# Optimization experiments

Measured on AMD Instinct MI355X. Metric: run time of the kernel, lower is better.

## Reference

```python
import jax, jax.numpy as jnp
import numpy as np

CUTOFF = 10.0
K = 32            # max_num_neighbors
NUM_GRAPHS = 64
ATOMS = 128
N = NUM_GRAPHS * ATOMS
HID = 128
FIL = 128
NG = 50           # num_gaussians
LAYERS = 6
MAX_Z = 100
PI = 3.14159265   # constant used verbatim in the torch source


def silu(x):
    return x * jax.nn.sigmoid(x)


def build_graph(pos, batch):
    """Dense cdist + per-node top-K neighbor selection (radius_graph_pure).
    Returns idx[i,k] = k-th nearest neighbor j of center i, and a validity mask.
    Torch edge (row, col) = (j, i): node j receives a message computed from x[i].
    """
    p = jax.lax.stop_gradient(pos)
    d2 = jnp.sum((p[:, None, :] - p[None, :, :]) ** 2, -1)          # [N,N]
    same = batch[:, None] == batch[None, :]
    eye = jnp.eye(p.shape[0], dtype=bool)
    valid = same & (d2 < CUTOFF * CUTOFF) & (~eye)
    dm = jnp.where(valid, d2, jnp.inf)
    neg, idx = jax.lax.top_k(-dm, K)                                 # [N,K]
    return idx, jnp.isfinite(neg)                                    # edge valid iff within mask


def setup_inputs() -> dict:
    key = jax.random.key(0)
    ks = jax.random.split(key, 20)
    s = 0.05
    inp = {
        "pos": jax.random.normal(ks[0], (N, 3), jnp.float32),
        "z": jax.random.randint(ks[1], (N,), 0, MAX_Z),
        "batch": jnp.repeat(jnp.arange(NUM_GRAPHS), ATOMS),
        # parameters (weights stored as [in, out])
        "emb": jax.random.normal(ks[2], (MAX_Z, HID), jnp.float32) * s,
        "mw1": jax.random.normal(ks[3], (LAYERS, NG, FIL), jnp.float32) * s,
        "mb1": jax.random.normal(ks[4], (LAYERS, FIL), jnp.float32) * s,
        "mw2": jax.random.normal(ks[5], (LAYERS, FIL, FIL), jnp.float32) * s,
        "mb2": jax.random.normal(ks[6], (LAYERS, FIL), jnp.float32) * s,
        "l1w": jax.random.normal(ks[7], (LAYERS, HID, FIL), jnp.float32) * s,
        "l1b": jax.random.normal(ks[8], (LAYERS, FIL), jnp.float32) * s,
        "l2w": jax.random.normal(ks[9], (LAYERS, FIL, HID), jnp.float32) * s,
        "l2b": jax.random.normal(ks[10], (LAYERS, HID), jnp.float32) * s,
        "ow1": jax.random.normal(ks[11], (HID, HID // 2), jnp.float32) * s,
        "ob1": jax.random.normal(ks[12], (HID // 2,), jnp.float32) * s,
        "ow2": jax.random.normal(ks[13], (HID // 2, 1), jnp.float32) * s,
        "ob2": jax.random.normal(ks[14], (1,), jnp.float32) * s,
    }
    return inp


def reference(pos, z, batch, emb, mw1, mb1, mw2, mb2, l1w, l1b, l2w, l2b, ow1, ob1, ow2, ob2):
    idx, evalid = build_graph(pos, batch)                 # [N,K], [N,K]
    ev = evalid.astype(pos.dtype)
    diff = pos[idx] - pos[:, None, :]                     # [N,K,3]
    d2e = jnp.sum(diff * diff, -1)
    dist = jnp.sqrt(jnp.where(evalid, d2e, 1.0))          # safe sqrt for masked edges
    offset = jnp.linspace(0.0, CUTOFF, NG)
    width = CUTOFF / (NG - 1)
    rbf = jnp.exp(-0.5 * ((dist[..., None] - offset) / width) ** 2)   # [N,K,NG]
    cval = 0.5 * (jnp.cos(dist * PI / CUTOFF) + 1.0)
    cval = cval * (dist < CUTOFF).astype(pos.dtype) * ev  # zero out invalid edges

    h = emb[z]                                            # [N,HID]
    flat_idx = idx.reshape(-1)                            # receivers (torch row)
    for l in range(LAYERS):
        W = silu(rbf @ mw1[l] + mb1[l]) @ mw2[l] + mb2[l]           # filter MLP
        W = W * cval[..., None]                                       # [N,K,FIL]
        xj = (h @ l1w[l] + l1b[l])[:, None, :]                        # sender = center i
        msg = (xj * W).reshape(N * K, FIL)
        agg = jax.ops.segment_sum(msg, flat_idx, num_segments=N)     # scatter_add at row
        h = h + silu(agg @ l2w[l] + l2b[l])

    out = (silu(h @ ow1 + ob1) @ ow2 + ob2)[:, 0]         # [N]
    return jax.ops.segment_sum(out, batch, num_segments=NUM_GRAPHS)  # [G]
```

## Files before the change

kernel.cpp:

```cpp
#include <hip/hip_runtime.h>
#include <math.h>

typedef unsigned short u16;
typedef unsigned int   u32;
typedef unsigned long long u64;

#define NATOMS 8192
#define GRAPHS 64
#define APG    128
#define KNN    32
#define NGAUSS 50
#define HID    128
#define LAYERS 6
#define NTAB   4096
#define SA     136
#define SW1    72
#define SH     132

typedef __attribute__((ext_vector_type(8))) short bf16x8;
typedef __attribute__((ext_vector_type(4))) float f32x4;

__device__ __forceinline__ float bf2f(u16 v) {
    return __uint_as_float(((u32)v) << 16);
}
__device__ __forceinline__ u16 f2bf(float f) {
    u32 u = __float_as_uint(f);
    u32 lsb = (u >> 16) & 1u;
    u += 0x7fffu + lsb;
    return (u16)(u >> 16);
}
__device__ __forceinline__ u32 pkbf(float lo, float hi) {
#if __has_builtin(__builtin_amdgcn_cvt_pk_bf16_f32)
    auto r = __builtin_amdgcn_cvt_pk_bf16_f32(lo, hi);
    u32 u; __builtin_memcpy(&u, &r, 4); return u;
#else
    return (u32)f2bf(lo) | ((u32)f2bf(hi) << 16);
#endif
}
__device__ __forceinline__ float silu_f(float x) {
    return x * __builtin_amdgcn_rcpf(1.0f + __expf(-x));
}
__device__ __forceinline__ bf16x8 ldfrag(const u16* p) {
    return *(const bf16x8*)__builtin_assume_aligned(p, 16);
}
__device__ __forceinline__ u64 shfl_xor_u64(u64 v, int mask) {
    u32 lo = (u32)v, hi = (u32)(v >> 32);
    lo = (u32)__shfl_xor((int)lo, mask, 64);
    hi = (u32)__shfl_xor((int)hi, mask, 64);
    return ((u64)hi << 32) | lo;
}
union U8 { bf16x8 v; u32 w[4]; };

__global__ void probe_kernel(const u16* __restrict__ raw, int* __restrict__ flag,
                             int* __restrict__ rev_cnt, float* __restrict__ gsum) {
    __shared__ int s;
    int t = threadIdx.x;
    if (t == 0) s = 0;
    __syncthreads();
    float x = bf2f(raw[2 * t]);
    if (!(fabsf(x) < 1000.0f)) atomicOr(&s, 1);
    for (int i = t; i < NATOMS; i += 256) rev_cnt[i] = 0;
    if (t < GRAPHS) gsum[t] = 0.0f;
    __syncthreads();
    if (t == 0) *flag = s;
}

#define NARR 10
struct IngestDesc {
    const void* src[NARR];
    void*       dst[NARR];
    int         n[NARR];
};

__global__ void ingest_kernel(IngestDesc d, const int* __restrict__ flag, int total) {
    int gid = blockIdx.x * blockDim.x + threadIdx.x;
    if (gid >= total) return;
    int a = 0, off = gid;
    while (off >= d.n[a]) { off -= d.n[a]; ++a; }
    bool f32in = (*flag != 0);
    float v = f32in ? ((const float*)d.src[a])[off]
                    : bf2f(((const u16*)d.src[a])[off]);
    ((float*)d.dst[a])[off] = v;
}

__global__ void prep_weights(const void* __restrict__ l1w, const void* __restrict__ l2w,
                             const void* __restrict__ mw2, const void* __restrict__ mw1,
                             u16* __restrict__ l1wt, u16* __restrict__ l2wt,
                             u16* __restrict__ mw2t, u16* __restrict__ mw1t,
                             const int* __restrict__ flag) {
    int gid = blockIdx.x * blockDim.x + threadIdx.x;
    bool f32in = (*flag != 0);
    if (gid < 3 * 98304) {
        int seg = gid / 98304;
        int t = gid % 98304;
        int l = t >> 14;
        int n = (t >> 7) & 127;
        int k = t & 127;
        const void* src = (seg == 0) ? l1w : ((seg == 1) ? l2w : mw2);
        u16* dst = (seg == 0) ? l1wt : ((seg == 1) ? l2wt : mw2t);
        int si = l * 16384 + k * 128 + n;
        float v = f32in ? ((const float*)src)[si] : bf2f(((const u16*)src)[si]);
        dst[t] = f2bf(v);
    } else {
        int t = gid - 3 * 98304;
        if (t < 49152) {
            int l = t >> 13;
            int n = (t >> 6) & 127;
            int k = t & 63;
            float v = 0.0f;
            if (k < 50) {
                int si = l * 6400 + k * 128 + n;
                v = f32in ? ((const float*)mw1)[si] : bf2f(((const u16*)mw1)[si]);
            }
            mw1t[t] = f2bf(v);
        }
    }
}

__launch_bounds__(256)
__global__ void build_graph_kernel(const float* __restrict__ pos,
                                   int* __restrict__ rev_cnt,
                                   int2* __restrict__ rev_si) {
    int wv = threadIdx.x >> 6, lane = threadIdx.x & 63;
    int t = blockIdx.x * 4 + wv;
    int tl = t & 127;
    int base = t & ~127;
    float cx = pos[t * 3 + 0];
    float cy = pos[t * 3 + 1];
    float cz = pos[t * 3 + 2];
    u64 key[2];
#pragma unroll
    for (int c = 0; c < 2; ++c) {
        int j = lane + c * 64;
        float jx = pos[(base + j) * 3 + 0];
        float jy = pos[(base + j) * 3 + 1];
        float jz = pos[(base + j) * 3 + 2];
        float dx = __fsub_rn(cx, jx);
        float dy = __fsub_rn(cy, jy);
        float dz = __fsub_rn(cz, jz);
        float d2 = __fadd_rn(__fadd_rn(__fmul_rn(dx, dx), __fmul_rn(dy, dy)),
                             __fmul_rn(dz, dz));
        bool valid = (j != tl) && (d2 < 100.0f);
        key[c] = valid ? ((((u64)__float_as_uint(d2)) << 32) | (u32)j) : ~0ULL;
    }
#pragma unroll
    for (int k = 2; k <= 128; k <<= 1) {
#pragma unroll
        for (int j = k >> 1; j > 0; j >>= 1) {
            if (j == 64) {
                u64 lo = key[0] < key[1] ? key[0] : key[1];
                u64 hi = key[0] < key[1] ? key[1] : key[0];
                key[0] = lo; key[1] = hi;
            } else {
#pragma unroll
                for (int r = 0; r < 2; ++r) {
                    u64 o = shfl_xor_u64(key[r], j);
                    u32 ii = (u32)(r * 64 + lane);
                    bool dir = ((ii & (u32)k) == 0);
                    bool lower = ((ii & (u32)j) == 0);
                    bool keep_min = (dir == lower);
                    bool less = key[r] < o;
                    key[r] = (less == keep_min) ? key[r] : o;
                }
            }
        }
    }
    if (lane < KNN) {
        u64 m = key[0];
        if (m != ~0ULL) {
            float d2 = __uint_as_float((u32)(m >> 32));
            float d = __fsqrt_rn(d2);
            if (d < 10.0f) {
                float u = d * ((float)(NTAB - 1) / 10.0f);
                int i0 = (int)(u + 0.5f);
                if (i0 > NTAB - 1) i0 = NTAB - 1;
                int jn = base + (int)(m & 0xffffffffu);
                int p = atomicAdd(&rev_cnt[jn], 1);
                rev_si[(size_t)jn * 128 + p] = make_int2(t, i0);
            }
        }
    }
}

__launch_bounds__(256)
__global__ void vtab_kernel(const u16* __restrict__ mw1t,
                            const u16* __restrict__ mw2t,
                            const float* __restrict__ b1,
                            const float* __restrict__ b2,
                            u32* __restrict__ pk) {
    __shared__ u16 s_t1[128 * SA];
    __shared__ u16 s_w1[128 * SW1];
    __shared__ u16 s_w2[128 * SA];
    int tid = threadIdx.x;
    int l = blockIdx.x / (NTAB / 128);
    int rbase = (blockIdx.x % (NTAB / 128)) * 128;
    {
        const uint4* g1 = (const uint4*)(mw1t + (size_t)l * 8192);
#pragma unroll
        for (int p = 0; p < 4; ++p) {
            int q = tid + p * 256;
            int row = q >> 3, c8 = (q & 7) * 8;
            *(uint4*)&s_w1[row * SW1 + c8] = g1[q];
        }
        const uint4* g2 = (const uint4*)(mw2t + (size_t)l * 16384);
#pragma unroll
        for (int p = 0; p < 8; ++p) {
            int q = tid + p * 256;
            int row = q >> 4, c8 = (q & 15) * 8;
            *(uint4*)&s_w2[row * SA + c8] = g2[q];
        }
    }
    __syncthreads();

    int wv = tid >> 6, lane = tid & 63;
    int quad = lane >> 4, lr = lane & 15;
    int m0 = wv * 32;

    {
        const float wgi = 49.0f / 10.0f;
        const float dstep = 10.0f / (float)(NTAB - 1);
        U8 afr[2][2];
#pragma unroll
        for (int mt = 0; mt < 2; ++mt) {
            float d = (float)(rbase + m0 + mt * 16 + lr) * dstep;
            float u = d * wgi;
#pragma unroll
            for (int kki = 0; kki < 2; ++kki) {
                float t0 = u - (float)(quad * 8) - (float)(kki * 32);
                float vj[8];
#pragma unroll
                for (int j = 0; j < 8; ++j) {
                    float tt = t0 - (float)j;
                    float e = __expf(-0.5f * tt * tt);
                    if (kki == 1 && (quad * 8 + j) >= 18) e = 0.0f;
                    vj[j] = e;
                }
#pragma unroll
                for (int p = 0; p < 4; ++p)
                    afr[mt][kki].w[p] = pkbf(vj[2 * p], vj[2 * p + 1]);
            }
        }
        f32x4 accA[2][8];
#pragma unroll
        for (int mt = 0; mt < 2; ++mt)
#pragma unroll
            for (int nt = 0; nt < 8; ++nt) accA[mt][nt] = (f32x4){0.f, 0.f, 0.f, 0.f};
#pragma unroll
        for (int kki = 0; kki < 2; ++kki) {
#pragma unroll
            for (int nt = 0; nt < 8; ++nt) {
                bf16x8 b = ldfrag(&s_w1[(nt * 16 + lr) * SW1 + kki * 32 + quad * 8]);
                accA[0][nt] = __builtin_amdgcn_mfma_f32_16x16x32_bf16(afr[0][kki].v, b, accA[0][nt], 0, 0, 0);
                accA[1][nt] = __builtin_amdgcn_mfma_f32_16x16x32_bf16(afr[1][kki].v, b, accA[1][nt], 0, 0, 0);
            }
        }
#pragma unroll
        for (int mt = 0; mt < 2; ++mt) {
            int r0 = m0 + mt * 16 + quad * 4;
            u16* tp0 = &s_t1[r0 * SA + lr];
#pragma unroll
            for (int nt = 0; nt < 8; ++nt) {
                int col = nt * 16;
                float bb = b1[l * 128 + col + lr];
                u32 p01 = pkbf(silu_f(accA[mt][nt][0] + bb),
                               silu_f(accA[mt][nt][1] + bb));
                u32 p23 = pkbf(silu_f(accA[mt][nt][2] + bb),
                               silu_f(accA[mt][nt][3] + bb));
                u16* tp = tp0 + col;
                tp[0]      = (u16)p01;
                tp[SA]     = (u16)(p01 >> 16);
                tp[2 * SA] = (u16)p23;
                tp[3 * SA] = (u16)(p23 >> 16);
            }
        }
    }

    {
        f32x4 accB[2][8];
#pragma unroll
        for (int mt = 0; mt < 2; ++mt)
#pragma unroll
            for (int nt = 0; nt < 8; ++nt) accB[mt][nt] = (f32x4){0.f, 0.f, 0.f, 0.f};
#pragma unroll
        for (int kk = 0; kk < 128; kk += 32) {
            bf16x8 a0 = ldfrag(&s_t1[(m0 + lr)      * SA + kk + quad * 8]);
            bf16x8 a1 = ldfrag(&s_t1[(m0 + 16 + lr) * SA + kk + quad * 8]);
#pragma unroll
            for (int nt = 0; nt < 8; ++nt) {
                bf16x8 b = ldfrag(&s_w2[(nt * 16 + lr) * SA + kk + quad * 8]);
                accB[0][nt] = __builtin_amdgcn_mfma_f32_16x16x32_bf16(a0, b, accB[0][nt], 0, 0, 0);
                accB[1][nt] = __builtin_amdgcn_mfma_f32_16x16x32_bf16(a1, b, accB[1][nt], 0, 0, 0);
            }
        }
        const float dstep = 10.0f / (float)(NTAB - 1);
#pragma unroll
        for (int mt = 0; mt < 2; ++mt) {
            int r0 = m0 + mt * 16 + quad * 4;
            float cv[4];
#pragma unroll
            for (int r = 0; r < 4; ++r) {
                float d = (float)(rbase + r0 + r) * dstep;
                cv[r] = 0.5f * (cosf(d * 3.14159265f / 10.0f) + 1.0f);
            }
#pragma unroll
            for (int nt = 0; nt < 8; ++nt) {
                int col = nt * 16 + lr;
                float bb = b2[l * 128 + col];
#pragma unroll
                for (int r = 0; r < 4; ++r) {
                    float val = (accB[mt][nt][r] + bb) * cv[r];
                    float oth = __shfl_xor(val, 1, 64);
                    if ((lr & 1) == 0) {
                        int row = rbase + r0 + r;
                        pk[((size_t)l * NTAB + row) * 64 + (col >> 1)] =
                            pkbf(val, oth);
                    }
                }
            }
        }
    }
}

__launch_bounds__(256)
__global__ void gemm0_kernel(const int* __restrict__ z,
                             const float* __restrict__ emb,
                             const u16* __restrict__ Bt,
                             const float* __restrict__ bias,
                             u16* __restrict__ xjb) {
    __shared__ u16 s_a[16 * SA];
    __shared__ float s_bias[128];
    int tid = threadIdx.x;
    int row0 = blockIdx.x * 16;
#pragma unroll
    for (int p = 0; p < 2; ++p) {
        int q = tid + p * 256;
        int r = q >> 5, c4 = (q & 31) * 4;
        const float* src = emb + (size_t)z[row0 + r] * 128;
        float4 v = *(const float4*)(src + c4);
        u32* d = (u32*)&s_a[r * SA + c4];
        d[0] = pkbf(v.x, v.y); d[1] = pkbf(v.z, v.w);
    }
    if (tid < 128) s_bias[tid] = bias[tid];
    __syncthreads();
    int wv = tid >> 6, lane = tid & 63;
    int quad = lane >> 4, lr = lane & 15;
    int n0 = wv * 32;
    f32x4 acc[2];
#pragma unroll
    for (int nt = 0; nt < 2; ++nt) acc[nt] = (f32x4){0.f, 0.f, 0.f, 0.f};
#pragma unroll
    for (int kk = 0; kk < 128; kk += 32) {
        bf16x8 a = ldfrag(&s_a[lr * SA + kk + quad * 8]);
#pragma unroll
        for (int nt = 0; nt < 2; ++nt) {
            bf16x8 b = ldfrag(Bt + (n0 + nt * 16 + lr) * 128 + kk + quad * 8);
            acc[nt] = __builtin_amdgcn_mfma_f32_16x16x32_bf16(a, b, acc[nt], 0, 0, 0);
        }
    }
#pragma unroll
    for (int nt = 0; nt < 2; ++nt)
#pragma unroll
        for (int r = 0; r < 4; ++r) {
            int col = n0 + nt * 16 + lr;
            xjb[(size_t)(row0 + quad * 4 + r) * 128 + col] =
                f2bf(acc[nt][r] + s_bias[col]);
        }
}

__launch_bounds__(256, 4)
__global__ void agg_kernel(const int* __restrict__ rev_cnt,
                           const int2* __restrict__ rev_si,
                           const u32* __restrict__ pk,
                           const u16* __restrict__ xjb,
                           float* __restrict__ agg) {
    int j = blockIdx.x * 4 + (threadIdx.x >> 6);
    int lane = threadIdx.x & 63;
    int deg = rev_cnt[j];
    const int2* si = rev_si + (size_t)j * 128;
    int c2 = lane * 2;
    float a0 = 0.f, a1 = 0.f, b0 = 0.f, b1 = 0.f;
    float c0 = 0.f, c1 = 0.f, d0 = 0.f, d1 = 0.f;
    int it = 0;
    for (; it + 8 <= deg; it += 8) {
        u32 t[8], x[8];
#pragma unroll
        for (int q = 0; q < 8; ++q) {
            int2 s = si[it + q];
            t[q] = pk[(size_t)s.y * 64 + lane];
            x[q] = *(const u32*)(xjb + (size_t)s.x * 128 + c2);
        }
#pragma unroll
        for (int q = 0; q < 8; ++q) {
            float v0 = bf2f((u16)t[q]) * bf2f((u16)x[q]);
            float v1 = bf2f((u16)(t[q] >> 16)) * bf2f((u16)(x[q] >> 16));
            switch (q & 3) {
                case 0: a0 += v0; a1 += v1; break;
                case 1: b0 += v0; b1 += v1; break;
                case 2: c0 += v0; c1 += v1; break;
                default: d0 += v0; d1 += v1; break;
            }
        }
    }
    for (; it + 4 <= deg; it += 4) {
        u32 t[4], x[4];
#pragma unroll
        for (int q = 0; q < 4; ++q) {
            int2 s = si[it + q];
            t[q] = pk[(size_t)s.y * 64 + lane];
            x[q] = *(const u32*)(xjb + (size_t)s.x * 128 + c2);
        }
#pragma unroll
        for (int q = 0; q < 4; ++q) {
            float v0 = bf2f((u16)t[q]) * bf2f((u16)x[q]);
            float v1 = bf2f((u16)(t[q] >> 16)) * bf2f((u16)(x[q] >> 16));
            if (q == 0) { a0 += v0; a1 += v1; }
            else if (q == 1) { b0 += v0; b1 += v1; }
            else if (q == 2) { c0 += v0; c1 += v1; }
            else { d0 += v0; d1 += v1; }
        }
    }
    for (; it < deg; ++it) {
        int2 s = si[it];
        u32 t = pk[(size_t)s.y * 64 + lane];
        u32 x = *(const u32*)(xjb + (size_t)s.x * 128 + c2);
        a0 += bf2f((u16)t) * bf2f((u16)x);
        a1 += bf2f((u16)(t >> 16)) * bf2f((u16)(x >> 16));
    }
    float2 r;
    r.x = (a0 + b0) + (c0 + d0);
    r.y = (a1 + b1) + (c1 + d1);
    *(float2*)(agg + (size_t)j * 128 + c2) = r;
}

template <int EMB, int LAST>
__launch_bounds__(256)
__global__ void layer_tail_kernel(const float* __restrict__ agg,
                                  float* __restrict__ h,
                                  const int* __restrict__ z,
                                  const float* __restrict__ emb,
                                  const u16* __restrict__ B2t,
                                  const float* __restrict__ b2,
                                  const u16* __restrict__ B1n,
                                  const float* __restrict__ b1n,
                                  u16* __restrict__ xjb) {
    __shared__ u16 s_ahi[16 * SA];
    __shared__ u16 s_alo[16 * SA];
    __shared__ float s_h[16 * SH];
    __shared__ float s_b2[128], s_b1[128];
    int tid = threadIdx.x;
    int row0 = blockIdx.x * 16;
#pragma unroll
    for (int p = 0; p < 2; ++p) {
        int q = tid + p * 256;
        int r = q >> 5, c4 = (q & 31) * 4;
        float4 v = *(const float4*)(agg + (size_t)(row0 + r) * 128 + c4);
        u32 h0 = pkbf(v.x, v.y), h1 = pkbf(v.z, v.w);
        u32* hd = (u32*)&s_ahi[r * SA + c4];
        hd[0] = h0; hd[1] = h1;
        u32 l0 = pkbf(v.x - bf2f((u16)h0), v.y - bf2f((u16)(h0 >> 16)));
        u32 l1 = pkbf(v.z - bf2f((u16)h1), v.w - bf2f((u16)(h1 >> 16)));
        u32* ld = (u32*)&s_alo[r * SA + c4];
        ld[0] = l0; ld[1] = l1;
    }
    if (tid < 128) {
        s_b2[tid] = b2[tid];
        if (!LAST) s_b1[tid] = b1n[tid];
    }
    __syncthreads();

    int wv = tid >> 6, lane = tid & 63;
    int quad = lane >> 4, lr = lane & 15;
    int n0 = wv * 32;

    f32x4 acc[2];
#pragma unroll
    for (int nt = 0; nt < 2; ++nt) acc[nt] = (f32x4){0.f, 0.f, 0.f, 0.f};
#pragma unroll
    for (int kk = 0; kk < 128; kk += 32) {
        bf16x8 ah = ldfrag(&s_ahi[lr * SA + kk + quad * 8]);
        bf16x8 al = ldfrag(&s_alo[lr * SA + kk + quad * 8]);
#pragma unroll
        for (int nt = 0; nt < 2; ++nt) {
            bf16x8 b = ldfrag(B2t + (n0 + nt * 16 + lr) * 128 + kk + quad * 8);
            acc[nt] = __builtin_amdgcn_mfma_f32_16x16x32_bf16(ah, b, acc[nt], 0, 0, 0);
            acc[nt] = __builtin_amdgcn_mfma_f32_16x16x32_bf16(al, b, acc[nt], 0, 0, 0);
        }
    }
#pragma unroll
    for (int nt = 0; nt < 2; ++nt)
#pragma unroll
        for (int r = 0; r < 4; ++r) {
            int row = quad * 4 + r;
            int col = n0 + nt * 16 + lr;
            size_t off = (size_t)(row0 + row) * 128 + col;
            float hold = EMB ? emb[(size_t)z[row0 + row] * 128 + col] : h[off];
            float hn = hold + silu_f(acc[nt][r] + s_b2[col]);
            h[off] = hn;
            s_h[row * SH + col] = hn;
        }
    if (!LAST) {
        __syncthreads();
        f32x4 ac2[2];
#pragma unroll
        for (int nt = 0; nt < 2; ++nt) ac2[nt] = (f32x4){0.f, 0.f, 0.f, 0.f};
#pragma unroll
        for (int kk = 0; kk < 128; kk += 32) {
            const float* ap = &s_h[lr * SH + kk + quad * 8];
            float4 v0 = *(const float4*)ap;
            float4 v1 = *(const float4*)(ap + 4);
            U8 a;
            a.w[0] = pkbf(v0.x, v0.y); a.w[1] = pkbf(v0.z, v0.w);
            a.w[2] = pkbf(v1.x, v1.y); a.w[3] = pkbf(v1.z, v1.w);
#pragma unroll
            for (int nt = 0; nt < 2; ++nt) {
                bf16x8 b = ldfrag(B1n + (n0 + nt * 16 + lr) * 128 + kk + quad * 8);
                ac2[nt] = __builtin_amdgcn_mfma_f32_16x16x32_bf16(a.v, b, ac2[nt], 0, 0, 0);
            }
        }
#pragma unroll
        for (int nt = 0; nt < 2; ++nt)
#pragma unroll
            for (int r = 0; r < 4; ++r) {
                int col = n0 + nt * 16 + lr;
                xjb[(size_t)(row0 + quad * 4 + r) * 128 + col] =
                    f2bf(ac2[nt][r] + s_b1[col]);
            }
    }
}

__launch_bounds__(256)
__global__ void head_kernel(const float* __restrict__ h,
                            const float* __restrict__ ow1,
                            const float* __restrict__ ob1,
                            const float* __restrict__ ow2,
                            const float* __restrict__ ob2,
                            float* __restrict__ gsum) {
    __shared__ __align__(16) float s_w[128 * 64];
    __shared__ __align__(16) float s_h[16 * 132];
    __shared__ float s_sum;
    int tid = threadIdx.x;
    int a0 = blockIdx.x * 16;
    if (tid == 0) s_sum = 0.0f;
    {
        const float4* src = (const float4*)ow1;
        float4* dst = (float4*)s_w;
#pragma unroll
        for (int p = 0; p < 8; ++p) dst[tid + p * 256] = src[tid + p * 256];
    }
    {
        const float4* src = (const float4*)(h + (size_t)a0 * 128);
#pragma unroll
        for (int p = 0; p < 2; ++p) {
            int q = tid + p * 256;
            int r = q >> 5, c4 = (q & 31) * 4;
            *(float4*)&s_h[r * 132 + c4] = src[q];
        }
    }
    __syncthreads();
    int atom = tid >> 4, cg = tid & 15;
    const float* hr = &s_h[atom * 132];
    const float4* w4 = (const float4*)s_w;
    float4 acc = {0.f, 0.f, 0.f, 0.f};
#pragma unroll 8
    for (int f = 0; f < 128; ++f) {
        float hv = hr[f];
        float4 w = w4[f * 16 + cg];
        acc.x += hv * w.x; acc.y += hv * w.y;
        acc.z += hv * w.z; acc.w += hv * w.w;
    }
    int c0 = cg * 4;
    float v = silu_f(acc.x + ob1[c0 + 0]) * ow2[c0 + 0]
            + silu_f(acc.y + ob1[c0 + 1]) * ow2[c0 + 1]
            + silu_f(acc.z + ob1[c0 + 2]) * ow2[c0 + 2]
            + silu_f(acc.w + ob1[c0 + 3]) * ow2[c0 + 3];
    v += __shfl_xor(v, 1, 64);
    v += __shfl_xor(v, 2, 64);
    v += __shfl_xor(v, 4, 64);
    v += __shfl_xor(v, 8, 64);
    if ((tid & 15) == 0) atomicAdd(&s_sum, v + ob2[0]);
    __syncthreads();
    if (tid == 0) atomicAdd(&gsum[a0 >> 7], s_sum);
}

__global__ void finalize_kernel(const float* __restrict__ gsum, void* __restrict__ out,
                                const int* __restrict__ flag) {
    int t = threadIdx.x;
    if (*flag) ((float*)out)[t] = gsum[t];
    else       ((u16*)out)[t]   = f2bf(gsum[t]);
}

extern "C" void kernel_launch(void* const* d_in, const int* in_sizes, int n_in,
                              void* d_out, int out_size, void* d_ws, size_t ws_size,
                              hipStream_t stream) {
    const void* pos  = d_in[0];
    const int*  z    = (const int*)d_in[1];
    const void* emb  = d_in[3];
    const void* mw1  = d_in[4];
    const void* mb1  = d_in[5];
    const void* mw2  = d_in[6];
    const void* mb2  = d_in[7];
    const void* l1w  = d_in[8];
    const void* l1b  = d_in[9];
    const void* l2w  = d_in[10];
    const void* l2b  = d_in[11];
    const void* ow1  = d_in[12];
    const void* ob1  = d_in[13];
    const void* ow2  = d_in[14];
    const void* ob2  = d_in[15];

    char* ws = (char*)d_ws;
    const size_t KB = 1024, MB = 1048576;
    int*   w_flag  = (int*)  (ws);
    float* c_pos   = (float*)(ws + 4   * KB);
    float* c_emb   = (float*)(ws + 112 * KB);
    float* c_mb1   = (float*)(ws + 168 * KB);
    float* c_mb2   = (float*)(ws + 176 * KB);
    float* c_l1b   = (float*)(ws + 184 * KB);
    float* c_l2b   = (float*)(ws + 192 * KB);
    float* c_ow1   = (float*)(ws + 200 * KB);
    float* c_ob1   = (float*)(ws + 236 * KB);
    float* c_ow2   = (float*)(ws + 240 * KB);
    float* c_ob2   = (float*)(ws + 244 * KB);
    float* w_gsum  = (float*)(ws + 248 * KB);
    u16*   c_l1wt  = (u16*)  (ws + 256 * KB);
    u16*   c_l2wt  = (u16*)  (ws + 448 * KB);
    u16*   c_mw2t  = (u16*)  (ws + 640 * KB);
    u16*   c_mw1t  = (u16*)  (ws + 832 * KB);
    int*   rev_cnt = (int*)  (ws + 2  * MB);
    int2*  rev_si  = (int2*) (ws + 3  * MB);
    float* w_h     = (float*)(ws + 11 * MB);
    u16*   w_xjb   = (u16*)  (ws + 15 * MB);
    float* w_agg   = (float*)(ws + 17 * MB);
    u32*   w_pk    = (u32*)  (ws + 21 * MB);

    probe_kernel<<<1, 256, 0, stream>>>((const u16*)emb, w_flag, rev_cnt, w_gsum);

    IngestDesc dsc;
    const void* srcs[NARR] = {pos, emb, mb1, mb2, l1b, l2b, ow1, ob1, ow2, ob2};
    void* dsts[NARR] = {c_pos, c_emb, c_mb1, c_mb2, c_l1b, c_l2b, c_ow1, c_ob1,
                        c_ow2, c_ob2};
    int ns_[NARR] = {24576, 12800, 768, 768, 768, 768, 8192, 64, 64, 1};
    int total = 0;
    for (int a = 0; a < NARR; ++a) {
        dsc.src[a] = srcs[a]; dsc.dst[a] = dsts[a]; dsc.n[a] = ns_[a];
        total += ns_[a];
    }
    ingest_kernel<<<(total + 255) / 256, 256, 0, stream>>>(dsc, w_flag, total);
    prep_weights<<<1344, 256, 0, stream>>>(l1w, l2w, mw2, mw1,
                                           c_l1wt, c_l2wt, c_mw2t, c_mw1t, w_flag);

    build_graph_kernel<<<NATOMS / 4, 256, 0, stream>>>(c_pos, rev_cnt, rev_si);
    vtab_kernel<<<LAYERS * NTAB / 128, 256, 0, stream>>>(
        c_mw1t, c_mw2t, c_mb1, c_mb2, w_pk);

    gemm0_kernel<<<NATOMS / 16, 256, 0, stream>>>(z, c_emb, c_l1wt, c_l1b, w_xjb);

    for (int l = 0; l < LAYERS; ++l) {
        agg_kernel<<<NATOMS / 4, 256, 0, stream>>>(
            rev_cnt, rev_si, w_pk + (size_t)l * NTAB * 64, w_xjb, w_agg);
        const u16* B2 = c_l2wt + (size_t)l * 16384;
        const float* b2 = c_l2b + (size_t)l * 128;
        const u16* B1n = c_l1wt + (size_t)(l + 1) * 16384;
        const float* b1n = c_l1b + (size_t)(l + 1) * 128;
        if (l == 0)
            layer_tail_kernel<1, 0><<<NATOMS / 16, 256, 0, stream>>>(
                w_agg, w_h, z, c_emb, B2, b2, B1n, b1n, w_xjb);
        else if (l < LAYERS - 1)
            layer_tail_kernel<0, 0><<<NATOMS / 16, 256, 0, stream>>>(
                w_agg, w_h, z, c_emb, B2, b2, B1n, b1n, w_xjb);
        else
            layer_tail_kernel<0, 1><<<NATOMS / 16, 256, 0, stream>>>(
                w_agg, w_h, z, c_emb, B2, b2, nullptr, nullptr, nullptr);
    }

    head_kernel<<<NATOMS / 16, 256, 0, stream>>>(w_h, c_ow1, c_ob1, c_ow2, c_ob2,
                                                 w_gsum);
    finalize_kernel<<<1, GRAPHS, 0, stream>>>(w_gsum, (void*)d_out, w_flag);
}
```

Baseline: 278.4 us.

## Fuse aggregation into layer tail, merge setup kernels, fold head and finalize

Merges ingest, weight prep and graph build into one setup kernel that reads pos directly. Each layer's gather-aggregate now runs inside the layer-tail GEMM kernel, so the fp32 agg buffer is never written to or read back from global memory. Ping-pong xjb buffers avoid read/write hazards. The output head and finalize step are folded into the last layer using a done-counter last-block pattern. This removes many launches and round trips, but the aggregation now runs with 512 blocks of 16 rows instead of 2048 blocks with one wave per node, which lowers parallelism for the latency-bound gather.

Result: slower. 295.6 us (+6.2%).

```diff
diff --git a/kernel.cpp b/kernel.cpp
--- a/kernel.cpp
+++ b/kernel.cpp
@@ -7,7 +7,6 @@
 
 #define NATOMS 8192
 #define GRAPHS 64
-#define APG    128
 #define KNN    32
 #define NGAUSS 50
 #define HID    128
@@ -49,10 +48,14 @@
     hi = (u32)__shfl_xor((int)hi, mask, 64);
     return ((u64)hi << 32) | lo;
 }
+__device__ __forceinline__ float ldf(const void* p, int i, bool f32in) {
+    return f32in ? ((const float*)p)[i] : bf2f(((const u16*)p)[i]);
+}
 union U8 { bf16x8 v; u32 w[4]; };
 
 __global__ void probe_kernel(const u16* __restrict__ raw, int* __restrict__ flag,
-                             int* __restrict__ rev_cnt, float* __restrict__ gsum) {
+                             int* __restrict__ rev_cnt, float* __restrict__ gsum,
+                             int* __restrict__ done_cnt) {
     __shared__ int s;
     int t = threadIdx.x;
     if (t == 0) s = 0;
@@ -61,123 +64,127 @@
     if (!(fabsf(x) < 1000.0f)) atomicOr(&s, 1);
     for (int i = t; i < NATOMS; i += 256) rev_cnt[i] = 0;
     if (t < GRAPHS) gsum[t] = 0.0f;
+    if (t == 0) *done_cnt = 0;
     __syncthreads();
     if (t == 0) *flag = s;
 }
 
-#define NARR 10
+#define NARR 9
 struct IngestDesc {
     const void* src[NARR];
     void*       dst[NARR];
     int         n[NARR];
 };
 
-__global__ void ingest_kernel(IngestDesc d, const int* __restrict__ flag, int total) {
-    int gid = blockIdx.x * blockDim.x + threadIdx.x;
-    if (gid >= total) return;
-    int a = 0, off = gid;
-    while (off >= d.n[a]) { off -= d.n[a]; ++a; }
-    bool f32in = (*flag != 0);
-    float v = f32in ? ((const float*)d.src[a])[off]
-                    : bf2f(((const u16*)d.src[a])[off]);
-    ((float*)d.dst[a])[off] = v;
-}
-
-__global__ void prep_weights(const void* __restrict__ l1w, const void* __restrict__ l2w,
+#define NB_BUILD 2048
+#define NB_PREP  1344
+
+__launch_bounds__(256)
+__global__ void setup_kernel(const void* __restrict__ pos,
+                             const void* __restrict__ l1w, const void* __restrict__ l2w,
                              const void* __restrict__ mw2, const void* __restrict__ mw1,
                              u16* __restrict__ l1wt, u16* __restrict__ l2wt,
                              u16* __restrict__ mw2t, u16* __restrict__ mw1t,
-                             const int* __restrict__ flag) {
-    int gid = blockIdx.x * blockDim.x + threadIdx.x;
+                             IngestDesc d, int total_ing,
+                             const int* __restrict__ flag,
+                             int* __restrict__ rev_cnt, int2* __restrict__ rev_si) {
+    int bid = blockIdx.x;
     bool f32in = (*flag != 0);
-    if (gid < 3 * 98304) {
-        int seg = gid / 98304;
-        int t = gid % 98304;
-        int l = t >> 14;
-        int n = (t >> 7) & 127;
-        int k = t & 127;
-        const void* src = (seg == 0) ? l1w : ((seg == 1) ? l2w : mw2);
-        u16* dst = (seg == 0) ? l1wt : ((seg == 1) ? l2wt : mw2t);
-        int si = l * 16384 + k * 128 + n;
-        float v = f32in ? ((const float*)src)[si] : bf2f(((const u16*)src)[si]);
-        dst[t] = f2bf(v);
+    if (bid < NB_BUILD) {
+        int wv = threadIdx.x >> 6, lane = threadIdx.x & 63;
+        int t = bid * 4 + wv;
+        int tl = t & 127;
+        int base = t & ~127;
+        float cx = ldf(pos, t * 3 + 0, f32in);
+        float cy = ldf(pos, t * 3 + 1, f32in);
+        float cz = ldf(pos, t * 3 + 2, f32in);
+        u64 key[2];
+#pragma unroll
+        for (int c = 0; c < 2; ++c) {
+            int j = lane + c * 64;
+            float jx = ldf(pos, (base + j) * 3 + 0, f32in);
+            float jy = ldf(pos, (base + j) * 3 + 1, f32in);
+            float jz = ldf(pos, (base + j) * 3 + 2, f32in);
+            float dx = __fsub_rn(cx, jx);
+            float dy = __fsub_rn(cy, jy);
+            float dz = __fsub_rn(cz, jz);
+            float d2 = __fadd_rn(__fadd_rn(__fmul_rn(dx, dx), __fmul_rn(dy, dy)),
+                                 __fmul_rn(dz, dz));
+            bool valid = (j != tl) && (d2 < 100.0f);
+            key[c] = valid ? ((((u64)__float_as_uint(d2)) << 32) | (u32)j) : ~0ULL;
+        }
+#pragma unroll
+        for (int k = 2; k <= 128; k <<= 1) {
+#pragma unroll
+            for (int j = k >> 1; j > 0; j >>= 1) {
+                if (j == 64) {
+                    u64 lo = key[0] < key[1] ? key[0] : key[1];
+                    u64 hi = key[0] < key[1] ? key[1] : key[0];
+                    key[0] = lo; key[1] = hi;
+                } else {
+#pragma unroll
+                    for (int r = 0; r < 2; ++r) {
+                        u64 o = shfl_xor_u64(key[r], j);
+                        u32 ii = (u32)(r * 64 + lane);
+                        bool dir = ((ii & (u32)k) == 0);
+                        bool lower = ((ii & (u32)j) == 0);
+                        bool keep_min = (dir == lower);
+                        bool less = key[r] < o;
+                        key[r] = (less == keep_min) ? key[r] : o;
+                    }
+                }
+            }
+        }
+        if (lane < KNN) {
+            u64 m = key[0];
+            if (m != ~0ULL) {
+                float d2 = __uint_as_float((u32)(m >> 32));
+                float dd = __fsqrt_rn(d2);
+                if (dd < 10.0f) {
+                    float u = dd * ((float)(NTAB - 1) / 10.0f);
+                    int i0 = (int)(u + 0.5f);
+                    if (i0 > NTAB - 1) i0 = NTAB - 1;
+                    int jn = base + (int)(m & 0xffffffffu);
+                    int p = atomicAdd(&rev_cnt[jn], 1);
+                    rev_si[(size_t)jn * 128 + p] = make_int2(t, i0);
+                }
+            }
+        }
+    } else if (bid < NB_BUILD + NB_PREP) {
+        int gid = (bid - NB_BUILD) * 256 + threadIdx.x;
+        if (gid < 3 * 98304) {
+            int seg = gid / 98304;
+            int tt = gid % 98304;
+            int l = tt >> 14;
+            int n = (tt >> 7) & 127;
+            int k = tt & 127;
+            const void* src = (seg == 0) ? l1w : ((seg == 1) ? l2w : mw2);
+            u16* dst = (seg == 0) ? l1wt : ((seg == 1) ? l2wt : mw2t);
+            int si = l * 16384 + k * 128 + n;
+            float v = f32in ? ((const float*)src)[si] : bf2f(((const u16*)src)[si]);
+            dst[tt] = f2bf(v);
+        } else {
+            int tt = gid - 3 * 98304;
+            if (tt < 49152) {
+                int l = tt >> 13;
+                int n = (tt >> 6) & 127;
+                int k = tt & 63;
+                float v = 0.0f;
+                if (k < 50) {
+                    int si = l * 6400 + k * 128 + n;
+                    v = f32in ? ((const float*)mw1)[si] : bf2f(((const u16*)mw1)[si]);
+                }
+                mw1t[tt] = f2bf(v);
+            }
+        }
     } else {
-        int t = gid - 3 * 98304;
-        if (t < 49152) {
-            int l = t >> 13;
-            int n = (t >> 6) & 127;
-            int k = t & 63;
-            float v = 0.0f;
-            if (k < 50) {
-                int si = l * 6400 + k * 128 + n;
-                v = f32in ? ((const float*)mw1)[si] : bf2f(((const u16*)mw1)[si]);
-            }
-            mw1t[t] = f2bf(v);
-        }
-    }
-}
-
-__launch_bounds__(256)
-__global__ void build_graph_kernel(const float* __restrict__ pos,
-                                   int* __restrict__ rev_cnt,
-                                   int2* __restrict__ rev_si) {
-    int wv = threadIdx.x >> 6, lane = threadIdx.x & 63;
-    int t = blockIdx.x * 4 + wv;
-    int tl = t & 127;
-    int base = t & ~127;
-    float cx = pos[t * 3 + 0];
-    float cy = pos[t * 3 + 1];
-    float cz = pos[t * 3 + 2];
-    u64 key[2];
-#pragma unroll
-    for (int c = 0; c < 2; ++c) {
-        int j = lane + c * 64;
-        float jx = pos[(base + j) * 3 + 0];
-        float jy = pos[(base + j) * 3 + 1];
-        float jz = pos[(base + j) * 3 + 2];
-        float dx = __fsub_rn(cx, jx);
-        float dy = __fsub_rn(cy, jy);
-        float dz = __fsub_rn(cz, jz);
-        float d2 = __fadd_rn(__fadd_rn(__fmul_rn(dx, dx), __fmul_rn(dy, dy)),
-                             __fmul_rn(dz, dz));
-        bool valid = (j != tl) && (d2 < 100.0f);
-        key[c] = valid ? ((((u64)__float_as_uint(d2)) << 32) | (u32)j) : ~0ULL;
-    }
-#pragma unroll
-    for (int k = 2; k <= 128; k <<= 1) {
-#pragma unroll
-        for (int j = k >> 1; j > 0; j >>= 1) {
-            if (j == 64) {
-                u64 lo = key[0] < key[1] ? key[0] : key[1];
-                u64 hi = key[0] < key[1] ? key[1] : key[0];
-                key[0] = lo; key[1] = hi;
-            } else {
-#pragma unroll
-                for (int r = 0; r < 2; ++r) {
-                    u64 o = shfl_xor_u64(key[r], j);
-                    u32 ii = (u32)(r * 64 + lane);
-                    bool dir = ((ii & (u32)k) == 0);
-                    bool lower = ((ii & (u32)j) == 0);
-                    bool keep_min = (dir == lower);
-                    bool less = key[r] < o;
-                    key[r] = (less == keep_min) ? key[r] : o;
-                }
-            }
-        }
-    }
-    if (lane < KNN) {
-        u64 m = key[0];
-        if (m != ~0ULL) {
-            float d2 = __uint_as_float((u32)(m >> 32));
-            float d = __fsqrt_rn(d2);
-            if (d < 10.0f) {
-                float u = d * ((float)(NTAB - 1) / 10.0f);
-                int i0 = (int)(u + 0.5f);
-                if (i0 > NTAB - 1) i0 = NTAB - 1;
-                int jn = base + (int)(m & 0xffffffffu);
-                int p = atomicAdd(&rev_cnt[jn], 1);
-                rev_si[(size_t)jn * 128 + p] = make_int2(t, i0);
-            }
+        int gid = (bid - NB_BUILD - NB_PREP) * 256 + threadIdx.x;
+        if (gid < total_ing) {
+            int a = 0, off = gid;
+            while (off >= d.n[a]) { off -= d.n[a]; ++a; }
+            float v = f32in ? ((const float*)d.src[a])[off]
+                            : bf2f(((const u16*)d.src[a])[off]);
+            ((float*)d.dst[a])[off] = v;
         }
     }
 }
@@ -274,7 +281,6 @@
             }
         }
     }
-
     {
         f32x4 accB[2][8];
 #pragma unroll
@@ -337,8 +343,8 @@
         int r = q >> 5, c4 = (q & 31) * 4;
         const float* src = emb + (size_t)z[row0 + r] * 128;
         float4 v = *(const float4*)(src + c4);
-        u32* d = (u32*)&s_a[r * SA + c4];
-        d[0] = pkbf(v.x, v.y); d[1] = pkbf(v.z, v.w);
+        u32* dd = (u32*)&s_a[r * SA + c4];
+        dd[0] = pkbf(v.x, v.y); dd[1] = pkbf(v.z, v.w);
     }
     if (tid < 128) s_bias[tid] = bias[tid];
     __syncthreads();
@@ -367,111 +373,118 @@
         }
 }
 
-__launch_bounds__(256, 4)
-__global__ void agg_kernel(const int* __restrict__ rev_cnt,
-                           const int2* __restrict__ rev_si,
-                           const u32* __restrict__ pk,
-                           const u16* __restrict__ xjb,
-                           float* __restrict__ agg) {
-    int j = blockIdx.x * 4 + (threadIdx.x >> 6);
-    int lane = threadIdx.x & 63;
-    int deg = rev_cnt[j];
-    const int2* si = rev_si + (size_t)j * 128;
-    int c2 = lane * 2;
-    float a0 = 0.f, a1 = 0.f, b0 = 0.f, b1 = 0.f;
-    float c0 = 0.f, c1 = 0.f, d0 = 0.f, d1 = 0.f;
-    int it = 0;
-    for (; it + 8 <= deg; it += 8) {
-        u32 t[8], x[8];
-#pragma unroll
-        for (int q = 0; q < 8; ++q) {
-            int2 s = si[it + q];
-            t[q] = pk[(size_t)s.y * 64 + lane];
-            x[q] = *(const u32*)(xjb + (size_t)s.x * 128 + c2);
-        }
-#pragma unroll
-        for (int q = 0; q < 8; ++q) {
-            float v0 = bf2f((u16)t[q]) * bf2f((u16)x[q]);
-            float v1 = bf2f((u16)(t[q] >> 16)) * bf2f((u16)(x[q] >> 16));
-            switch (q & 3) {
-                case 0: a0 += v0; a1 += v1; break;
-                case 1: b0 += v0; b1 += v1; break;
-                case 2: c0 += v0; c1 += v1; break;
-                default: d0 += v0; d1 += v1; break;
-            }
-        }
-    }
-    for (; it + 4 <= deg; it += 4) {
-        u32 t[4], x[4];
-#pragma unroll
-        for (int q = 0; q < 4; ++q) {
-            int2 s = si[it + q];
-            t[q] = pk[(size_t)s.y * 64 + lane];
-            x[q] = *(const u32*)(xjb + (size_t)s.x * 128 + c2);
-        }
-#pragma unroll
-        for (int q = 0; q < 4; ++q) {
-            float v0 = bf2f((u16)t[q]) * bf2f((u16)x[q]);
-            float v1 = bf2f((u16)(t[q] >> 16)) * bf2f((u16)(x[q] >> 16));
-            if (q == 0) { a0 += v0; a1 += v1; }
-            else if (q == 1) { b0 += v0; b1 += v1; }
-            else if (q == 2) { c0 += v0; c1 += v1; }
-            else { d0 += v0; d1 += v1; }
-        }
-    }
-    for (; it < deg; ++it) {
-        int2 s = si[it];
-        u32 t = pk[(size_t)s.y * 64 + lane];
-        u32 x = *(const u32*)(xjb + (size_t)s.x * 128 + c2);
-        a0 += bf2f((u16)t) * bf2f((u16)x);
-        a1 += bf2f((u16)(t >> 16)) * bf2f((u16)(x >> 16));
-    }
-    float2 r;
-    r.x = (a0 + b0) + (c0 + d0);
-    r.y = (a1 + b1) + (c1 + d1);
-    *(float2*)(agg + (size_t)j * 128 + c2) = r;
-}
-
 template <int EMB, int LAST>
 __launch_bounds__(256)
-__global__ void layer_tail_kernel(const float* __restrict__ agg,
-                                  float* __restrict__ h,
-                                  const int* __restrict__ z,
-                                  const float* __restrict__ emb,
-                                  const u16* __restrict__ B2t,
-                                  const float* __restrict__ b2,
-                                  const u16* __restrict__ B1n,
-                                  const float* __restrict__ b1n,
-                                  u16* __restrict__ xjb) {
+__global__ void layer_fused_kernel(const int* __restrict__ rev_cnt,
+                                   const int2* __restrict__ rev_si,
+                                   const u32* __restrict__ pk,
+                                   const u16* __restrict__ xjb_in,
+                                   float* __restrict__ h,
+                                   const int* __restrict__ z,
+                                   const float* __restrict__ emb,
+                                   const u16* __restrict__ B2t,
+                                   const float* __restrict__ b2,
+                                   const u16* __restrict__ B1n,
+                                   const float* __restrict__ b1n,
+                                   u16* __restrict__ xjb_out,
+                                   const float* __restrict__ ow1,
+                                   const float* __restrict__ ob1,
+                                   const float* __restrict__ ow2,
+                                   const float* __restrict__ ob2,
+                                   float* __restrict__ gsum,
+                                   int* __restrict__ done_cnt,
+                                   void* __restrict__ out,
+                                   const int* __restrict__ flag) {
     __shared__ u16 s_ahi[16 * SA];
     __shared__ u16 s_alo[16 * SA];
     __shared__ float s_h[16 * SH];
     __shared__ float s_b2[128], s_b1[128];
+    __shared__ float s_w[LAST ? 128 * 64 : 1];
+    __shared__ float s_sum;
+    __shared__ int s_last;
     int tid = threadIdx.x;
     int row0 = blockIdx.x * 16;
-#pragma unroll
-    for (int p = 0; p < 2; ++p) {
-        int q = tid + p * 256;
-        int r = q >> 5, c4 = (q & 31) * 4;
-        float4 v = *(const float4*)(agg + (size_t)(row0 + r) * 128 + c4);
-        u32 h0 = pkbf(v.x, v.y), h1 = pkbf(v.z, v.w);
-        u32* hd = (u32*)&s_ahi[r * SA + c4];
-        hd[0] = h0; hd[1] = h1;
-        u32 l0 = pkbf(v.x - bf2f((u16)h0), v.y - bf2f((u16)(h0 >> 16)));
-        u32 l1 = pkbf(v.z - bf2f((u16)h1), v.w - bf2f((u16)(h1 >> 16)));
-        u32* ld = (u32*)&s_alo[r * SA + c4];
-        ld[0] = l0; ld[1] = l1;
-    }
+    int wv = tid >> 6, lane = tid & 63;
+
     if (tid < 128) {
         s_b2[tid] = b2[tid];
         if (!LAST) s_b1[tid] = b1n[tid];
     }
+    if (LAST) {
+        if (tid == 0) s_sum = 0.0f;
+        const float4* src = (const float4*)ow1;
+        float4* dst = (float4*)s_w;
+#pragma unroll
+        for (int p = 0; p < 8; ++p) dst[tid + p * 256] = src[tid + p * 256];
+    }
+
+    {
+        int c2 = lane * 2;
+        for (int rr = 0; rr < 4; ++rr) {
+            int row = wv * 4 + rr;
+            int j = row0 + row;
+            int deg = rev_cnt[j];
+            const int2* si = rev_si + (size_t)j * 128;
+            float a0 = 0.f, a1 = 0.f, b0 = 0.f, b1v = 0.f;
+            float c0 = 0.f, c1 = 0.f, d0 = 0.f, d1 = 0.f;
+            int it = 0;
+            for (; it + 8 <= deg; it += 8) {
+                u32 tq[8], xq[8];
+#pragma unroll
+                for (int q = 0; q < 8; ++q) {
+                    int2 s = si[it + q];
+                    tq[q] = pk[(size_t)s.y * 64 + lane];
+                    xq[q] = *(const u32*)(xjb_in + (size_t)s.x * 128 + c2);
+                }
+#pragma unroll
+                for (int q = 0; q < 8; ++q) {
+                    float v0 = bf2f((u16)tq[q]) * bf2f((u16)xq[q]);
+                    float v1 = bf2f((u16)(tq[q] >> 16)) * bf2f((u16)(xq[q] >> 16));
+                    switch (q & 3) {
+                        case 0: a0 += v0; a1 += v1; break;
+                        case 1: b0 += v0; b1v += v1; break;
+                        case 2: c0 += v0; c1 += v1; break;
+                        default: d0 += v0; d1 += v1; break;
+                    }
+                }
+            }
+            for (; it + 4 <= deg; it += 4) {
+                u32 tq[4], xq[4];
+#pragma unroll
+                for (int q = 0; q < 4; ++q) {
+                    int2 s = si[it + q];
+                    tq[q] = pk[(size_t)s.y * 64 + lane];
+                    xq[q] = *(const u32*)(xjb_in + (size_t)s.x * 128 + c2);
+                }
+#pragma unroll
+                for (int q = 0; q < 4; ++q) {
+                    float v0 = bf2f((u16)tq[q]) * bf2f((u16)xq[q]);
+                    float v1 = bf2f((u16)(tq[q] >> 16)) * bf2f((u16)(xq[q] >> 16));
+                    if (q == 0) { a0 += v0; a1 += v1; }
+                    else if (q == 1) { b0 += v0; b1v += v1; }
+                    else if (q == 2) { c0 += v0; c1 += v1; }
+                    else { d0 += v0; d1 += v1; }
+                }
+            }
+            for (; it < deg; ++it) {
+                int2 s = si[it];
+                u32 tq = pk[(size_t)s.y * 64 + lane];
+                u32 xq = *(const u32*)(xjb_in + (size_t)s.x * 128 + c2);
+                a0 += bf2f((u16)tq) * bf2f((u16)xq);
+                a1 += bf2f((u16)(tq >> 16)) * bf2f((u16)(xq >> 16));
+            }
+            float sx = (a0 + b0) + (c0 + d0);
+            float sy = (a1 + b1v) + (c1 + d1);
+            u32 hp = pkbf(sx, sy);
+            u32 lp = pkbf(sx - bf2f((u16)hp), sy - bf2f((u16)(hp >> 16)));
+            *(u32*)&s_ahi[row * SA + c2] = hp;
+            *(u32*)&s_alo[row * SA + c2] = lp;
+        }
+    }
     __syncthreads();
 
-    int wv = tid >> 6, lane = tid & 63;
     int quad = lane >> 4, lr = lane & 15;
     int n0 = wv * 32;
-
     f32x4 acc[2];
 #pragma unroll
     for (int nt = 0; nt < 2; ++nt) acc[nt] = (f32x4){0.f, 0.f, 0.f, 0.f};
@@ -495,11 +508,12 @@
             size_t off = (size_t)(row0 + row) * 128 + col;
             float hold = EMB ? emb[(size_t)z[row0 + row] * 128 + col] : h[off];
             float hn = hold + silu_f(acc[nt][r] + s_b2[col]);
-            h[off] = hn;
+            if (!LAST) h[off] = hn;
             s_h[row * SH + col] = hn;
         }
+    __syncthreads();
+
     if (!LAST) {
-        __syncthreads();
         f32x4 ac2[2];
 #pragma unroll
         for (int nt = 0; nt < 2; ++nt) ac2[nt] = (f32x4){0.f, 0.f, 0.f, 0.f};
@@ -522,71 +536,47 @@
 #pragma unroll
             for (int r = 0; r < 4; ++r) {
                 int col = n0 + nt * 16 + lr;
-                xjb[(size_t)(row0 + quad * 4 + r) * 128 + col] =
+                xjb_out[(size_t)(row0 + quad * 4 + r) * 128 + col] =
                     f2bf(ac2[nt][r] + s_b1[col]);
             }
-    }
-}
-
-__launch_bounds__(256)
-__global__ void head_kernel(const float* __restrict__ h,
-                            const float* __restrict__ ow1,
-                            const float* __restrict__ ob1,
-                            const float* __restrict__ ow2,
-                            const float* __restrict__ ob2,
-                            float* __restrict__ gsum) {
-    __shared__ __align__(16) float s_w[128 * 64];
-    __shared__ __align__(16) float s_h[16 * 132];
-    __shared__ float s_sum;
-    int tid = threadIdx.x;
-    int a0 = blockIdx.x * 16;
-    if (tid == 0) s_sum = 0.0f;
-    {
-        const float4* src = (const float4*)ow1;
-        float4* dst = (float4*)s_w;
-#pragma unroll
-        for (int p = 0; p < 8; ++p) dst[tid + p * 256] = src[tid + p * 256];
-    }
-    {
-        const float4* src = (const float4*)(h + (size_t)a0 * 128);
-#pragma unroll
-        for (int p = 0; p < 2; ++p) {
-            int q = tid + p * 256;
-            int r = q >> 5, c4 = (q & 31) * 4;
-            *(float4*)&s_h[r * 132 + c4] = src[q];
-        }
-    }
-    __syncthreads();
-    int atom = tid >> 4, cg = tid & 15;
-    const float* hr = &s_h[atom * 132];
-    const float4* w4 = (const float4*)s_w;
-    float4 acc = {0.f, 0.f, 0.f, 0.f};
+    } else {
+        int atom = tid >> 4, cg = tid & 15;
+        const float* hr = &s_h[atom * SH];
+        const float4* w4 = (const float4*)s_w;
+        float4 a4 = {0.f, 0.f, 0.f, 0.f};
 #pragma unroll 8
-    for (int f = 0; f < 128; ++f) {
-        float hv = hr[f];
-        float4 w = w4[f * 16 + cg];
-        acc.x += hv * w.x; acc.y += hv * w.y;
-        acc.z += hv * w.z; acc.w += hv * w.w;
-    }
-    int c0 = cg * 4;
-    float v = silu_f(acc.x + ob1[c0 + 0]) * ow2[c0 + 0]
-            + silu_f(acc.y + ob1[c0 + 1]) * ow2[c0 + 1]
-            + silu_f(acc.z + ob1[c0 + 2]) * ow2[c0 + 2]
-            + silu_f(acc.w + ob1[c0 + 3]) * ow2[c0 + 3];
-    v += __shfl_xor(v, 1, 64);
-    v += __shfl_xor(v, 2, 64);
-    v += __shfl_xor(v, 4, 64);
-    v += __shfl_xor(v, 8, 64);
-    if ((tid & 15) == 0) atomicAdd(&s_sum, v + ob2[0]);
-    __syncthreads();
-    if (tid == 0) atomicAdd(&gsum[a0 >> 7], s_sum);
-}
-
-__global__ void finalize_kernel(const float* __restrict__ gsum, void* __restrict__ out,
-                                const int* __restrict__ flag) {
-    int t = threadIdx.x;
-    if (*flag) ((float*)out)[t] = gsum[t];
-    else       ((u16*)out)[t]   = f2bf(gsum[t]);
+        for (int f = 0; f < 128; ++f) {
+            float hv = hr[f];
+            float4 w = w4[f * 16 + cg];
+            a4.x += hv * w.x; a4.y += hv * w.y;
+            a4.z += hv * w.z; a4.w += hv * w.w;
+        }
+        int c0i = cg * 4;
+        float v = silu_f(a4.x + ob1[c0i + 0]) * ow2[c0i + 0]
+                + silu_f(a4.y + ob1[c0i + 1]) * ow2[c0i + 1]
+                + silu_f(a4.z + ob1[c0i + 2]) * ow2[c0i + 2]
+                + silu_f(a4.w + ob1[c0i + 3]) * ow2[c0i + 3];
+        v += __shfl_xor(v, 1, 64);
+        v += __shfl_xor(v, 2, 64);
+        v += __shfl_xor(v, 4, 64);
+        v += __shfl_xor(v, 8, 64);
+        if ((tid & 15) == 0) atomicAdd(&s_sum, v + ob2[0]);
+        __syncthreads();
+        if (tid == 0) {
+            atomicAdd(&gsum[row0 >> 7], s_sum);
+            __threadfence();
+            int tk = __hip_atomic_fetch_add(done_cnt, 1, __ATOMIC_ACQ_REL,
+                                            __HIP_MEMORY_SCOPE_AGENT);
+            s_last = (tk == (NATOMS / 16) - 1);
+        }
+        __syncthreads();
+        if (s_last && tid < GRAPHS) {
+            float g = __hip_atomic_load(&gsum[tid], __ATOMIC_RELAXED,
+                                        __HIP_MEMORY_SCOPE_AGENT);
+            if (*flag) ((float*)out)[tid] = g;
+            else       ((u16*)out)[tid]   = f2bf(g);
+        }
+    }
 }
 
 extern "C" void kernel_launch(void* const* d_in, const int* in_sizes, int n_in,
@@ -611,7 +601,7 @@
     char* ws = (char*)d_ws;
     const size_t KB = 1024, MB = 1048576;
     int*   w_flag  = (int*)  (ws);
-    float* c_pos   = (float*)(ws + 4   * KB);
+    int*   w_done  = (int*)  (ws + 64);
     float* c_emb   = (float*)(ws + 112 * KB);
     float* c_mb1   = (float*)(ws + 168 * KB);
     float* c_mb2   = (float*)(ws + 176 * KB);
@@ -629,51 +619,55 @@
     int*   rev_cnt = (int*)  (ws + 2  * MB);
     int2*  rev_si  = (int2*) (ws + 3  * MB);
     float* w_h     = (float*)(ws + 11 * MB);
-    u16*   w_xjb   = (u16*)  (ws + 15 * MB);
-    float* w_agg   = (float*)(ws + 17 * MB);
+    u16*   w_xjbA  = (u16*)  (ws + 15 * MB);
+    u16*   w_xjbB  = (u16*)  (ws + 17 * MB);
     u32*   w_pk    = (u32*)  (ws + 21 * MB);
 
-    probe_kernel<<<1, 256, 0, stream>>>((const u16*)emb, w_flag, rev_cnt, w_gsum);
+    probe_kernel<<<1, 256, 0, stream>>>((const u16*)emb, w_flag, rev_cnt,
+                                        w_gsum, w_done);
 
     IngestDesc dsc;
-    const void* srcs[NARR] = {pos, emb, mb1, mb2, l1b, l2b, ow1, ob1, ow2, ob2};
-    void* dsts[NARR] = {c_pos, c_emb, c_mb1, c_mb2, c_l1b, c_l2b, c_ow1, c_ob1,
+    const void* srcs[NARR] = {emb, mb1, mb2, l1b, l2b, ow1, ob1, ow2, ob2};
+    void* dsts[NARR] = {c_emb, c_mb1, c_mb2, c_l1b, c_l2b, c_ow1, c_ob1,
                         c_ow2, c_ob2};
-    int ns_[NARR] = {24576, 12800, 768, 768, 768, 768, 8192, 64, 64, 1};
+    int ns_[NARR] = {12800, 768, 768, 768, 768, 8192, 64, 64, 1};
     int total = 0;
     for (int a = 0; a < NARR; ++a) {
         dsc.src[a] = srcs[a]; dsc.dst[a] = dsts[a]; dsc.n[a] = ns_[a];
         total += ns_[a];
     }
-    ingest_kernel<<<(total + 255) / 256, 256, 0, stream>>>(dsc, w_flag, total);
-    prep_weights<<<1344, 256, 0, stream>>>(l1w, l2w, mw2, mw1,
-                                           c_l1wt, c_l2wt, c_mw2t, c_mw1t, w_flag);
-
-    build_graph_kernel<<<NATOMS / 4, 256, 0, stream>>>(c_pos, rev_cnt, rev_si);
+    int nb_ing = (total + 255) / 256;
+    setup_kernel<<<NB_BUILD + NB_PREP + nb_ing, 256, 0, stream>>>(
+        pos, l1w, l2w, mw2, mw1, c_l1wt, c_l2wt, c_mw2t, c_mw1t,
+        dsc, total, w_flag, rev_cnt, rev_si);
+
     vtab_kernel<<<LAYERS * NTAB / 128, 256, 0, stream>>>(
         c_mw1t, c_mw2t, c_mb1, c_mb2, w_pk);
 
-    gemm0_kernel<<<NATOMS / 16, 256, 0, stream>>>(z, c_emb, c_l1wt, c_l1b, w_xjb);
+    gemm0_kernel<<<NATOMS / 16, 256, 0, stream>>>(z, c_emb, c_l1wt, c_l1b, w_xjbA);
 
     for (int l = 0; l < LAYERS; ++l) {
-        agg_kernel<<<NATOMS / 4, 256, 0, stream>>>(
-            rev_cnt, rev_si, w_pk + (size_t)l * NTAB * 64, w_xjb, w_agg);
+        u16* xin  = (l & 1) ? w_xjbB : w_xjbA;
+        u16* xout = (l & 1) ? w_xjbA : w_xjbB;
         const u16* B2 = c_l2wt + (size_t)l * 16384;
         const float* b2 = c_l2b + (size_t)l * 128;
         const u16* B1n = c_l1wt + (size_t)(l + 1) * 16384;
         const float* b1n = c_l1b + (size_t)(l + 1) * 128;
+        const u32* pkl = w_pk + (size_t)l * NTAB * 64;
         if (l == 0)
-            layer_tail_kernel<1, 0><<<NATOMS / 16, 256, 0, stream>>>(
-                w_agg, w_h, z, c_emb, B2, b2, B1n, b1n, w_xjb);
+            layer_fused_kernel<1, 0><<<NATOMS / 16, 256, 0, stream>>>(
+                rev_cnt, rev_si, pkl, xin, w_h, z, c_emb, B2, b2, B1n, b1n, xout,
+                nullptr, nullptr, nullptr, nullptr, nullptr, nullptr, nullptr,
+                nullptr);
         else if (l < LAYERS - 1)
-            layer_tail_kernel<0, 0><<<NATOMS / 16, 256, 0, stream>>>(
-                w_agg, w_h, z, c_emb, B2, b2, B1n, b1n, w_xjb);
+            layer_fused_kernel<0, 0><<<NATOMS / 16, 256, 0, stream>>>(
+                rev_cnt, rev_si, pkl, xin, w_h, z, c_emb, B2, b2, B1n, b1n, xout,
+                nullptr, nullptr, nullptr, nullptr, nullptr, nullptr, nullptr,
+                nullptr);
         else
-            layer_tail_kernel<0, 1><<<NATOMS / 16, 256, 0, stream>>>(
-                w_agg, w_h, z, c_emb, B2, b2, nullptr, nullptr, nullptr);
-    }
-
-    head_kernel<<<NATOMS / 16, 256, 0, stream>>>(w_h, c_ow1, c_ob1, c_ow2, c_ob2,
-                                                 w_gsum);
-    finalize_kernel<<<1, GRAPHS, 0, stream>>>(w_gsum, (void*)d_out, w_flag);
-}
+            layer_fused_kernel<0, 1><<<NATOMS / 16, 256, 0, stream>>>(
+                rev_cnt, rev_si, pkl, xin, w_h, z, c_emb, B2, b2, nullptr,
+                nullptr, nullptr, c_ow1, c_ob1, c_ow2, c_ob2, w_gsum, w_done,
+                d_out, w_flag);
+    }
+}
```
